# Performance work log

Hardware: AMD Instinct MI355X
Metric: run time of the kernel (lower is better)

Reference implementation:

```python
import jax, jax.numpy as jnp
from jax import lax
import numpy as np

CONF_THRES = 0.55
IOU_THRES = 0.45
MAX_DET = 1000
MAX_WH = 7680.0   # class offset for class-aware NMS (agnostic=False)
K = 4096          # NMS candidate cap (yolov5 max_nms analogue, jit-static)
IMG = 640         # letterboxed network input size
B, N, NC = 16, 25200, 80


def setup_inputs() -> dict:
    key = jax.random.key(0)
    k1, k2, k3, k4 = jax.random.split(key, 4)
    cxcy = jax.random.uniform(k1, (B, N, 2), jnp.float32, 0.0, IMG)
    wh = jax.random.uniform(k2, (B, N, 2), jnp.float32, 2.0, 120.0)
    obj = jax.random.uniform(k3, (B, N, 1), jnp.float32) ** 4
    cls = jax.random.uniform(k4, (B, N, NC), jnp.float32)
    pred = jnp.concatenate([cxcy, wh, obj, cls], axis=-1)  # [B, N, 5+NC]
    return {"pred": pred, "img0_h": 1080, "img0_w": 1920}


def xywh2xyxy(x):
    cx, cy, w, h = x[..., 0], x[..., 1], x[..., 2], x[..., 3]
    return jnp.stack([cx - w / 2, cy - h / 2, cx + w / 2, cy + h / 2], axis=-1)


def box_iou(a, b):
    # a: [K,4], b: [K,4] xyxy -> [K,K]
    lt = jnp.maximum(a[:, None, :2], b[None, :, :2])
    rb = jnp.minimum(a[:, None, 2:], b[None, :, 2:])
    wh = jnp.clip(rb - lt, 0.0)
    inter = wh[..., 0] * wh[..., 1]
    area_a = (a[:, 2] - a[:, 0]) * (a[:, 3] - a[:, 1])
    area_b = (b[:, 2] - b[:, 0]) * (b[:, 3] - b[:, 1])
    return inter / (area_a[:, None] + area_b[None, :] - inter + 1e-7)


def _nms_image(p, img0_h, img0_w):
    # p: [N, 5+NC]
    obj = p[:, 4]
    cls_conf = p[:, 5:] * obj[:, None]          # conf = obj * cls
    conf = cls_conf.max(axis=-1)
    cls_id = cls_conf.argmax(axis=-1)
    valid = (obj > CONF_THRES) & (conf > CONF_THRES)
    score = jnp.where(valid, conf, -1.0)
    # top-K candidates, sorted by confidence (descending)
    top_scores, top_idx = lax.top_k(score, K)
    boxes = xywh2xyxy(p[top_idx, :4])           # [K,4]
    cl = cls_id[top_idx].astype(p.dtype)        # [K]
    iou = box_iou(boxes + cl[:, None] * MAX_WH, boxes + cl[:, None] * MAX_WH)
    idx = jnp.arange(K)
    keep0 = top_scores > 0.0

    def body(i, keep):
        # suppress i if a higher-scoring kept box overlaps it too much
        sup = jnp.any(keep & (idx < i) & (iou[:, i] > IOU_THRES))
        return keep.at[i].set(keep[i] & ~sup)

    keep = lax.fori_loop(0, K, body, keep0)
    kept_score = jnp.where(keep, top_scores, -1.0)
    fs, fi = lax.top_k(kept_score, MAX_DET)
    fb = boxes[fi]                              # [MAX_DET,4]
    fc = cl[fi]
    fvalid = fs > 0.0
    # scale_boxes: letterboxed 640x640 -> original img0
    gain = min(IMG / img0_h, IMG / img0_w)
    pad_x = (IMG - img0_w * gain) / 2
    pad_y = (IMG - img0_h * gain) / 2
    fb = (fb - jnp.array([pad_x, pad_y, pad_x, pad_y], fb.dtype)) / gain
    fb = jnp.clip(fb, 0.0, jnp.array([img0_w, img0_h, img0_w, img0_h], fb.dtype))
    fb = jnp.round(fb)
    det = jnp.concatenate([fb, fs[:, None], fc[:, None]], axis=-1)  # [MAX_DET,6]
    return jnp.where(fvalid[:, None], det, 0.0)


def reference(pred, img0_h, img0_w):
    return jax.vmap(lambda p: _nms_image(p, img0_h, img0_w))(pred)
```

## Files before the change

### kernel.cpp

```cpp
#include <hip/hip_runtime.h>

#define BB 16
#define NN 25200
#define NC 80
#define ROWL 85
#define KTOP 4096
#define MAXDET 1000
#define CONF_T 0.55f
#define IOU_T 0.45f
#define MAX_WH_F 7680.0f
#define CNT_STRIDE 32
#define PCNT_STRIDE 16
#define CCAP 256
#define NBIN 2048

#define OFF_CNT   81920
#define OFF_KCNT  83968
#define OFF_BUCK  86016
#define OFF_KEPT  2707456
#define ZERO_WORDS 21504

__global__ void zero_kernel(unsigned int* __restrict__ w) {
  w[blockIdx.x * 256 + threadIdx.x] = 0u;
}

__global__ __launch_bounds__(256) void score_kernel(const float* __restrict__ pred,
                             unsigned long long* __restrict__ buckets,
                             unsigned int* __restrict__ pcnt,
                             unsigned int* __restrict__ cnt) {
  const int b = blockIdx.y;
  const int lane = threadIdx.x & 63;
  const int a0 = blockIdx.x * 256 + (threadIdx.x & ~63);
  const int a = a0 + lane;
  const int g = lane >> 4;
  const int gl = lane & 15;
  const float* __restrict__ pb = pred + (size_t)b * NN * ROWL;
  float obj = 0.0f;
  if (a < NN) obj = pb[(size_t)a * ROWL + 4];
  unsigned long long mask = __ballot(obj > CONF_T);
  unsigned int nvacc = 0;
  while (mask) {
    int s0 = __ffsll(mask) - 1; mask &= mask - 1;
    int s1 = -1, s2 = -1, s3 = -1;
    if (mask) { s1 = __ffsll(mask) - 1; mask &= mask - 1; }
    if (mask) { s2 = __ffsll(mask) - 1; mask &= mask - 1; }
    if (mask) { s3 = __ffsll(mask) - 1; mask &= mask - 1; }
    const int sg = (g == 0) ? s0 : (g == 1) ? s1 : (g == 2) ? s2 : s3;
    const bool act = (sg >= 0);
    const int srow = act ? sg : s0;
    const int aa = a0 + srow;
    const float objg = __shfl(obj, srow, 64);
    const float* __restrict__ row = pb + (size_t)aa * ROWL;
    float best = -1.0f; int bi = gl;
    #pragma unroll
    for (int t = 0; t < 5; ++t) {
      float v = row[5 + gl + 16 * t] * objg;
      if (v > best) { best = v; bi = gl + 16 * t; }
    }
    #pragma unroll
    for (int off = 1; off <= 8; off <<= 1) {
      float ov = __shfl_xor(best, off, 64);
      int oi = __shfl_xor(bi, off, 64);
      if (ov > best || (ov == best && oi < bi)) { best = ov; bi = oi; }
    }
    bool emit = act && (gl == 0) && (best > CONF_T);
    if (emit) {
      unsigned long long key =
          ((unsigned long long)__float_as_uint(best) << 32) |
          ((unsigned long long)((~(unsigned)aa) & 0xFFFFu) << 16) |
          (unsigned long long)(unsigned)bi;
      unsigned int slot = atomicAdd(&pcnt[(b * NC + bi) * PCNT_STRIDE], 1u);
      if (slot < CCAP)
        buckets[((size_t)(b * NC + bi) << 8) + slot] = key;
    }
    unsigned long long em = __ballot(emit);
    if (lane == 0) nvacc += (unsigned int)__popcll(em);
  }
  if (lane == 0 && nvacc)
    atomicAdd(&cnt[b * CNT_STRIDE], nvacc);
}

__device__ __forceinline__ bool iou_sup(float ax1, float ay1, float ax2, float ay2,
                                        float aar, float bx1, float by1, float bx2,
                                        float by2, float bar) {
  float ltx = fmaxf(ax1, bx1), lty = fmaxf(ay1, by1);
  float rbx = fminf(ax2, bx2), rby = fminf(ay2, by2);
  float wv = rbx - ltx; wv = wv > 0.0f ? wv : 0.0f;
  float hv = rby - lty; hv = hv > 0.0f ? hv : 0.0f;
  float inter = wv * hv;
  float iou = inter / (aar + bar - inter + 1e-7f);
  return iou > IOU_T;
}

__global__ __launch_bounds__(64) void class_nms_kernel(
    const float* __restrict__ pred,
    const unsigned long long* __restrict__ buckets,
    const unsigned int* __restrict__ pcnt,
    const unsigned int* __restrict__ cnt,
    unsigned long long* __restrict__ kept,
    unsigned int* __restrict__ kcnt) {
  const int c = blockIdx.x;
  const int b = blockIdx.y;
  const int lane = threadIdx.x;
  unsigned int pc = pcnt[(b * NC + c) * PCNT_STRIDE];
  int n_c = (int)(pc < (unsigned)CCAP ? pc : (unsigned)CCAP);
  const unsigned long long* __restrict__ bk = buckets + ((size_t)(b * NC + c) << 8);
  const float* __restrict__ pb = pred + (size_t)b * NN * ROWL;
  const float offc = (float)c * MAX_WH_F;
  const int count = (int)cnt[b * CNT_STRIDE];

  if (n_c == 0) return;

  if (n_c <= 64 && count <= KTOP) {
    unsigned long long v0 = (lane < n_c) ? bk[lane] : 0ull;
    for (int k2 = 2; k2 <= 64; k2 <<= 1) {
      for (int j = k2 >> 1; j >= 1; j >>= 1) {
        unsigned long long vo = __shfl_xor(v0, j, 64);
        bool desc = ((lane & k2) == 0);
        bool low = ((lane & j) == 0);
        if ((desc == low) ? (vo > v0) : (vo < v0)) v0 = vo;
      }
    }
    float x1 = 0.f, y1 = 0.f, x2 = 0.f, y2 = 0.f, aar = 0.f;
    const bool inr = (lane < n_c);
    if (inr) {
      unsigned int lo = (unsigned int)v0;
      int aa = (int)((~(lo >> 16)) & 0xFFFFu);
      const float* row = pb + (size_t)aa * ROWL;
      float cx = row[0], cy = row[1], w2 = row[2], h2 = row[3];
      x1 = (cx - w2 / 2.0f) + offc;
      y1 = (cy - h2 / 2.0f) + offc;
      x2 = (cx + w2 / 2.0f) + offc;
      y2 = (cy + h2 / 2.0f) + offc;
      aar = (x2 - x1) * (y2 - y1);
    }
    unsigned long long rowreg = 0ull;
    for (int i2 = 0; i2 < n_c; ++i2) {
      float bx1 = __shfl(x1, i2, 64), by1 = __shfl(y1, i2, 64);
      float bx2 = __shfl(x2, i2, 64), by2 = __shfl(y2, i2, 64);
      float bar = __shfl(aar, i2, 64);
      bool sup = inr && (lane > i2) &&
                 iou_sup(bx1, by1, bx2, by2, bar, x1, y1, x2, y2, aar);
      unsigned long long rm = __ballot(sup);
      if (lane == i2) rowreg = rm;
    }
    unsigned long long cand = (n_c >= 64) ? ~0ull : ((1ull << n_c) - 1ull);
    unsigned long long keepm = 0ull;
    while (cand) {
      int i = __ffsll(cand) - 1;
      keepm |= (1ull << i);
      unsigned long long rowi = __shfl(rowreg, i, 64);
      cand &= ~rowi;
      cand &= ~(1ull << i);
    }
    int keep0 = (int)((keepm >> lane) & 1ull);
    unsigned long long m0 = __ballot(keep0 != 0);
    int tot = (int)__popcll(m0);
    unsigned int base3 = 0;
    if (lane == 0) base3 = atomicAdd(&kcnt[b * CNT_STRIDE], (unsigned int)tot);
    base3 = (unsigned int)__shfl((int)base3, 0, 64);
    if (keep0) {
      unsigned int slot = base3 + (unsigned int)__popcll(m0 & ((1ull << lane) - 1ull));
      if (slot < (unsigned)KTOP) kept[(size_t)b * KTOP + slot] = v0;
    }
    return;
  }

  unsigned long long v[4];
  #pragma unroll
  for (int r = 0; r < 4; ++r) {
    int e = (r << 6) + lane;
    v[r] = (e < n_c) ? bk[e] : 0ull;
  }
  if (count > KTOP) {
    unsigned long long T = 0ull;
    for (int bit = 63; bit >= 0; --bit) {
      unsigned long long T2 = T | (1ull << bit);
      int cge = 0;
      for (int c2 = 0; c2 < NC; ++c2) {
        unsigned int p2 = pcnt[(b * NC + c2) * PCNT_STRIDE];
        int n2 = (int)(p2 < (unsigned)CCAP ? p2 : (unsigned)CCAP);
        const unsigned long long* bk2 = buckets + ((size_t)(b * NC + c2) << 8);
        for (int base2 = 0; base2 < n2; base2 += 64) {
          int i = base2 + lane;
          bool ge = (i < n2) && (bk2[i] >= T2);
          cge += (int)__popcll(__ballot(ge));
        }
      }
      if (cge >= KTOP) T = T2;
    }
    #pragma unroll
    for (int r = 0; r < 4; ++r) if (v[r] < T) v[r] = 0ull;
    n_c = 0;
    #pragma unroll
    for (int r = 0; r < 4; ++r) n_c += (int)__popcll(__ballot(v[r] != 0ull));
    if (n_c == 0) return;
  }
  for (int k2 = 2; k2 <= 256; k2 <<= 1) {
    if (k2 == 256) {
      #pragma unroll
      for (int r = 0; r < 2; ++r) {
        unsigned e = (unsigned)((r << 6) + lane);
        bool desc = ((e & k2) == 0);
        unsigned long long lo_ = v[r], hi_ = v[r + 2];
        bool sw = desc ? (lo_ < hi_) : (lo_ > hi_);
        v[r] = sw ? hi_ : lo_; v[r + 2] = sw ? lo_ : hi_;
      }
    }
    if (k2 >= 128) {
      #pragma unroll
      for (int rr = 0; rr < 2; ++rr) {
        int r = rr * 2;
        unsigned e = (unsigned)((r << 6) + lane);
        bool desc = ((e & k2) == 0);
        unsigned long long lo_ = v[r], hi_ = v[r + 1];
        bool sw = desc ? (lo_ < hi_) : (lo_ > hi_);
        v[r] = sw ? hi_ : lo_; v[r + 1] = sw ? lo_ : hi_;
      }
    }
    int j0 = (k2 >> 1) < 32 ? (k2 >> 1) : 32;
    for (int j = j0; j >= 1; j >>= 1) {
      #pragma unroll
      for (int r = 0; r < 4; ++r) {
        unsigned e = (unsigned)((r << 6) + lane);
        unsigned long long vo = __shfl_xor(v[r], j, 64);
        bool desc = ((e & k2) == 0);
        bool low = ((e & j) == 0);
        if ((desc == low) ? (vo > v[r]) : (vo < v[r])) v[r] = vo;
      }
    }
  }
  float x1r[4], y1r[4], x2r[4], y2r[4], ar[4];
  int keepr[4];
  #pragma unroll
  for (int r = 0; r < 4; ++r) {
    int e = (r << 6) + lane;
    keepr[r] = 0; x1r[r] = 0.f; y1r[r] = 0.f; x2r[r] = 0.f; y2r[r] = 0.f; ar[r] = 0.f;
    if (e < n_c) {
      unsigned int lo = (unsigned int)v[r];
      int aa = (int)((~(lo >> 16)) & 0xFFFFu);
      const float* row = pb + (size_t)aa * ROWL;
      float cx = row[0], cy = row[1], w2 = row[2], h2 = row[3];
      x1r[r] = (cx - w2 / 2.0f) + offc;
      y1r[r] = (cy - h2 / 2.0f) + offc;
      x2r[r] = (cx + w2 / 2.0f) + offc;
      y2r[r] = (cy + h2 / 2.0f) + offc;
      ar[r] = (x2r[r] - x1r[r]) * (y2r[r] - y1r[r]);
      keepr[r] = 1;
    }
  }
  for (int i2 = 0; i2 < n_c; ++i2) {
    int ci = i2 >> 6, li = i2 & 63;
    int ki; float bx1v, by1v, bx2v, by2v, bav;
    #define BCAST(R) { ki = __shfl(keepr[R], li, 64); bx1v = __shfl(x1r[R], li, 64); \
                       by1v = __shfl(y1r[R], li, 64); bx2v = __shfl(x2r[R], li, 64); \
                       by2v = __shfl(y2r[R], li, 64); bav = __shfl(ar[R], li, 64); }
    switch (ci) {
      case 0: BCAST(0); break;
      case 1: BCAST(1); break;
      case 2: BCAST(2); break;
      default: BCAST(3); break;
    }
    #undef BCAST
    if (!ki) continue;
    #pragma unroll
    for (int r = 0; r < 4; ++r) {
      int e = (r << 6) + lane;
      if (keepr[r] && e > i2 &&
          iou_sup(bx1v, by1v, bx2v, by2v, bav, x1r[r], y1r[r], x2r[r], y2r[r], ar[r]))
        keepr[r] = 0;
    }
  }
  unsigned long long m[4];
  int tot = 0;
  #pragma unroll
  for (int r = 0; r < 4; ++r) {
    m[r] = __ballot(keepr[r] != 0);
    tot += (int)__popcll(m[r]);
  }
  unsigned int base3 = 0;
  if (lane == 0) base3 = atomicAdd(&kcnt[b * CNT_STRIDE], (unsigned int)tot);
  base3 = (unsigned int)__shfl((int)base3, 0, 64);
  unsigned int start = base3;
  #pragma unroll
  for (int r = 0; r < 4; ++r) {
    if (keepr[r]) {
      unsigned int slot = start + (unsigned int)__popcll(m[r] & ((1ull << lane) - 1ull));
      if (slot < (unsigned)KTOP) kept[(size_t)b * KTOP + slot] = v[r];
    }
    start += (unsigned int)__popcll(m[r]);
  }
}

__global__ __launch_bounds__(1024) void finalize_kernel(
    const float* __restrict__ pred,
    const unsigned long long* __restrict__ kept,
    const unsigned int* __restrict__ kcnt,
    const int* __restrict__ ihp, const int* __restrict__ iwp,
    float* __restrict__ out) {
  __shared__ unsigned int hist[NBIN];
  __shared__ unsigned int sufx[NBIN];
  __shared__ unsigned int curs[NBIN];
  __shared__ unsigned int scanbuf[1024];
  __shared__ unsigned long long skey[KTOP];
  const int b = blockIdx.x;
  const int tid = threadIdx.x;
  unsigned int kcr = kcnt[b * CNT_STRIDE];
  const int kc = (int)(kcr < (unsigned)KTOP ? kcr : (unsigned)KTOP);
  const unsigned long long* __restrict__ kb = kept + (size_t)b * KTOP;

  for (int i = tid; i < NBIN; i += 1024) hist[i] = 0u;
  __syncthreads();

  unsigned long long myk[4];
  int myb[4];
  #pragma unroll
  for (int r = 0; r < 4; ++r) {
    int i = tid + (r << 10);
    myb[r] = -1; myk[r] = 0ull;
    if (i < kc) {
      unsigned long long k = kb[i];
      int bin = (int)((k >> 44) & (unsigned long long)(NBIN - 1));
      myk[r] = k; myb[r] = bin;
      atomicAdd(&hist[bin], 1u);
    }
  }
  __syncthreads();

  unsigned int h0 = hist[2 * tid], h1 = hist[2 * tid + 1];
  unsigned int val = h0 + h1;
  scanbuf[tid] = val;
  __syncthreads();
  for (int off = 1; off < 1024; off <<= 1) {
    unsigned int add = (tid + off < 1024) ? scanbuf[tid + off] : 0u;
    __syncthreads();
    val += add;
    scanbuf[tid] = val;
    __syncthreads();
  }
  unsigned int excl = val - (h0 + h1);
  sufx[2 * tid] = excl + h1;
  sufx[2 * tid + 1] = excl;
  curs[2 * tid] = excl + h1;
  curs[2 * tid + 1] = excl;
  __syncthreads();

  #pragma unroll
  for (int r = 0; r < 4; ++r) {
    if (myb[r] >= 0) {
      unsigned int p = atomicAdd(&curs[myb[r]], 1u);
      skey[p] = myk[r];
    }
  }
  __syncthreads();

  const int h = ihp[0], w3 = iwp[0];
  const double gd = fmin(640.0 / (double)h, 640.0 / (double)w3);
  const float gain = (float)gd;
  const float padx = (float)((640.0 - (double)w3 * gd) * 0.5);
  const float pady = (float)((640.0 - (double)h * gd) * 0.5);
  const float wf = (float)w3, hf = (float)h;
  #pragma unroll
  for (int r = 0; r < 4; ++r) {
    if (myb[r] >= 0) {
      unsigned long long k = myk[r];
      unsigned int gstart = sufx[myb[r]];
      unsigned int gcnt = hist[myb[r]];
      unsigned int rank = gstart;
      for (unsigned int j = 0; j < gcnt; ++j)
        rank += (skey[gstart + j] > k) ? 1u : 0u;
      if (rank < MAXDET) {
        unsigned int lo = (unsigned int)k;
        int aa = (int)((~(lo >> 16)) & 0xFFFFu);
        int cls = (int)(lo & 0xFFFFu);
        float score = __uint_as_float((unsigned int)(k >> 32));
        const float* row = pred + ((size_t)b * NN + aa) * ROWL;
        float cx = row[0], cy = row[1], wd = row[2], ht = row[3];
        float x1 = cx - wd / 2.0f, y1 = cy - ht / 2.0f;
        float x2 = cx + wd / 2.0f, y2 = cy + ht / 2.0f;
        x1 = rintf(fminf(fmaxf((x1 - padx) / gain, 0.0f), wf));
        y1 = rintf(fminf(fmaxf((y1 - pady) / gain, 0.0f), hf));
        x2 = rintf(fminf(fmaxf((x2 - padx) / gain, 0.0f), wf));
        y2 = rintf(fminf(fmaxf((y2 - pady) / gain, 0.0f), hf));
        float* o = out + ((size_t)b * MAXDET + (int)rank) * 6;
        o[0] = x1; o[1] = y1; o[2] = x2; o[3] = y2;
        o[4] = score; o[5] = (float)cls;
      }
    }
  }
  for (int i = kc + tid; i < MAXDET; i += 1024) {
    float* o = out + ((size_t)b * MAXDET + i) * 6;
    o[0] = 0.0f; o[1] = 0.0f; o[2] = 0.0f; o[3] = 0.0f; o[4] = 0.0f; o[5] = 0.0f;
  }
}

extern "C" void kernel_launch(void* const* d_in, const int* in_sizes, int n_in,
                              void* d_out, int out_size, void* d_ws, size_t ws_size,
                              hipStream_t stream) {
  const float* pred = (const float*)d_in[0];
  const int* ih = (const int*)d_in[1];
  const int* iw = (const int*)d_in[2];
  float* out = (float*)d_out;
  char* ws = (char*)d_ws;

  unsigned int* pcnt = (unsigned int*)ws;
  unsigned int* cnt = (unsigned int*)(ws + OFF_CNT);
  unsigned int* kcnt = (unsigned int*)(ws + OFF_KCNT);
  unsigned long long* buckets = (unsigned long long*)(ws + OFF_BUCK);
  unsigned long long* kept = (unsigned long long*)(ws + OFF_KEPT);

  zero_kernel<<<ZERO_WORDS / 256, 256, 0, stream>>>((unsigned int*)ws);
  dim3 sgrid((NN + 255) / 256, BB);
  score_kernel<<<sgrid, 256, 0, stream>>>(pred, buckets, pcnt, cnt);
  dim3 cgrid(NC, BB);
  class_nms_kernel<<<cgrid, 64, 0, stream>>>(pred, buckets, pcnt, cnt, kept, kcnt);
  finalize_kernel<<<BB, 1024, 0, stream>>>(pred, kept, kcnt, ih, iw, out);
}
```

Measured before the change: 74.15 us.

## Coarsen score and class-NMS blocks, shrink counter padding, use wave-shuffle scan

Each score-kernel wave now handles four 64-anchor segments, so the grid drops to 25 blocks per image. The class NMS kernel packs four classes into one 256-thread block. The per-class counter stride shrinks, which reduces the workspace that must be zeroed. The finalize kernel's barrier-heavy suffix scan is replaced by a wave shuffle scan plus a small cross-wave combine. Together these aim to cut launch and block overhead, zeroing traffic and barrier count, at the cost of less parallelism in the score pass and more atomic contention on counters placed closer together.

```diff
diff --git a/kernel.cpp b/kernel.cpp
--- a/kernel.cpp
+++ b/kernel.cpp
@@ -10,15 +10,15 @@
 #define IOU_T 0.45f
 #define MAX_WH_F 7680.0f
 #define CNT_STRIDE 32
-#define PCNT_STRIDE 16
+#define PCNT_STRIDE 4
 #define CCAP 256
 #define NBIN 2048
 
-#define OFF_CNT   81920
-#define OFF_KCNT  83968
-#define OFF_BUCK  86016
-#define OFF_KEPT  2707456
-#define ZERO_WORDS 21504
+#define OFF_CNT   20480
+#define OFF_KCNT  22528
+#define OFF_BUCK  24576
+#define OFF_KEPT  2646016
+#define ZERO_WORDS 6144
 
 __global__ void zero_kernel(unsigned int* __restrict__ w) {
   w[blockIdx.x * 256 + threadIdx.x] = 0u;
@@ -30,51 +30,56 @@
                              unsigned int* __restrict__ cnt) {
   const int b = blockIdx.y;
   const int lane = threadIdx.x & 63;
-  const int a0 = blockIdx.x * 256 + (threadIdx.x & ~63);
-  const int a = a0 + lane;
+  const int w = threadIdx.x >> 6;
   const int g = lane >> 4;
   const int gl = lane & 15;
   const float* __restrict__ pb = pred + (size_t)b * NN * ROWL;
-  float obj = 0.0f;
-  if (a < NN) obj = pb[(size_t)a * ROWL + 4];
-  unsigned long long mask = __ballot(obj > CONF_T);
   unsigned int nvacc = 0;
-  while (mask) {
-    int s0 = __ffsll(mask) - 1; mask &= mask - 1;
-    int s1 = -1, s2 = -1, s3 = -1;
-    if (mask) { s1 = __ffsll(mask) - 1; mask &= mask - 1; }
-    if (mask) { s2 = __ffsll(mask) - 1; mask &= mask - 1; }
-    if (mask) { s3 = __ffsll(mask) - 1; mask &= mask - 1; }
-    const int sg = (g == 0) ? s0 : (g == 1) ? s1 : (g == 2) ? s2 : s3;
-    const bool act = (sg >= 0);
-    const int srow = act ? sg : s0;
-    const int aa = a0 + srow;
-    const float objg = __shfl(obj, srow, 64);
-    const float* __restrict__ row = pb + (size_t)aa * ROWL;
-    float best = -1.0f; int bi = gl;
-    #pragma unroll
-    for (int t = 0; t < 5; ++t) {
-      float v = row[5 + gl + 16 * t] * objg;
-      if (v > best) { best = v; bi = gl + 16 * t; }
-    }
-    #pragma unroll
-    for (int off = 1; off <= 8; off <<= 1) {
-      float ov = __shfl_xor(best, off, 64);
-      int oi = __shfl_xor(bi, off, 64);
-      if (ov > best || (ov == best && oi < bi)) { best = ov; bi = oi; }
-    }
-    bool emit = act && (gl == 0) && (best > CONF_T);
-    if (emit) {
-      unsigned long long key =
-          ((unsigned long long)__float_as_uint(best) << 32) |
-          ((unsigned long long)((~(unsigned)aa) & 0xFFFFu) << 16) |
-          (unsigned long long)(unsigned)bi;
-      unsigned int slot = atomicAdd(&pcnt[(b * NC + bi) * PCNT_STRIDE], 1u);
-      if (slot < CCAP)
-        buckets[((size_t)(b * NC + bi) << 8) + slot] = key;
-    }
-    unsigned long long em = __ballot(emit);
-    if (lane == 0) nvacc += (unsigned int)__popcll(em);
+  for (int t = 0; t < 4; ++t) {
+    const int seg = blockIdx.x * 16 + w * 4 + t;
+    const int a0 = seg * 64;
+    if (a0 >= NN) break;
+    const int a = a0 + lane;
+    float obj = 0.0f;
+    if (a < NN) obj = pb[(size_t)a * ROWL + 4];
+    unsigned long long mask = __ballot(obj > CONF_T);
+    while (mask) {
+      int s0 = __ffsll(mask) - 1; mask &= mask - 1;
+      int s1 = -1, s2 = -1, s3 = -1;
+      if (mask) { s1 = __ffsll(mask) - 1; mask &= mask - 1; }
+      if (mask) { s2 = __ffsll(mask) - 1; mask &= mask - 1; }
+      if (mask) { s3 = __ffsll(mask) - 1; mask &= mask - 1; }
+      const int sg = (g == 0) ? s0 : (g == 1) ? s1 : (g == 2) ? s2 : s3;
+      const bool act = (sg >= 0);
+      const int srow = act ? sg : s0;
+      const int aa = a0 + srow;
+      const float objg = __shfl(obj, srow, 64);
+      const float* __restrict__ row = pb + (size_t)aa * ROWL;
+      float best = -1.0f; int bi = gl;
+      #pragma unroll
+      for (int u = 0; u < 5; ++u) {
+        float v = row[5 + gl + 16 * u] * objg;
+        if (v > best) { best = v; bi = gl + 16 * u; }
+      }
+      #pragma unroll
+      for (int off = 1; off <= 8; off <<= 1) {
+        float ov = __shfl_xor(best, off, 64);
+        int oi = __shfl_xor(bi, off, 64);
+        if (ov > best || (ov == best && oi < bi)) { best = ov; bi = oi; }
+      }
+      bool emit = act && (gl == 0) && (best > CONF_T);
+      if (emit) {
+        unsigned long long key =
+            ((unsigned long long)__float_as_uint(best) << 32) |
+            ((unsigned long long)((~(unsigned)aa) & 0xFFFFu) << 16) |
+            (unsigned long long)(unsigned)bi;
+        unsigned int slot = atomicAdd(&pcnt[(b * NC + bi) * PCNT_STRIDE], 1u);
+        if (slot < CCAP)
+          buckets[((size_t)(b * NC + bi) << 8) + slot] = key;
+      }
+      unsigned long long em = __ballot(emit);
+      if (lane == 0) nvacc += (unsigned int)__popcll(em);
+    }
   }
   if (lane == 0 && nvacc)
     atomicAdd(&cnt[b * CNT_STRIDE], nvacc);
@@ -92,16 +97,16 @@
   return iou > IOU_T;
 }
 
-__global__ __launch_bounds__(64) void class_nms_kernel(
+__global__ __launch_bounds__(256) void class_nms_kernel(
     const float* __restrict__ pred,
     const unsigned long long* __restrict__ buckets,
     const unsigned int* __restrict__ pcnt,
     const unsigned int* __restrict__ cnt,
     unsigned long long* __restrict__ kept,
     unsigned int* __restrict__ kcnt) {
-  const int c = blockIdx.x;
+  const int c = blockIdx.x * 4 + (threadIdx.x >> 6);
   const int b = blockIdx.y;
-  const int lane = threadIdx.x;
+  const int lane = threadIdx.x & 63;
   unsigned int pc = pcnt[(b * NC + c) * PCNT_STRIDE];
   int n_c = (int)(pc < (unsigned)CCAP ? pc : (unsigned)CCAP);
   const unsigned long long* __restrict__ bk = buckets + ((size_t)(b * NC + c) << 8);
@@ -301,15 +306,17 @@
   __shared__ unsigned int hist[NBIN];
   __shared__ unsigned int sufx[NBIN];
   __shared__ unsigned int curs[NBIN];
-  __shared__ unsigned int scanbuf[1024];
+  __shared__ unsigned int wsum[16], woff[16];
   __shared__ unsigned long long skey[KTOP];
   const int b = blockIdx.x;
   const int tid = threadIdx.x;
+  const int lane = tid & 63;
+  const int w = tid >> 6;
   unsigned int kcr = kcnt[b * CNT_STRIDE];
   const int kc = (int)(kcr < (unsigned)KTOP ? kcr : (unsigned)KTOP);
   const unsigned long long* __restrict__ kb = kept + (size_t)b * KTOP;
 
-  for (int i = tid; i < NBIN; i += 1024) hist[i] = 0u;
+  hist[2 * tid] = 0u; hist[2 * tid + 1] = 0u;
   __syncthreads();
 
   unsigned long long myk[4];
@@ -328,17 +335,22 @@
   __syncthreads();
 
   unsigned int h0 = hist[2 * tid], h1 = hist[2 * tid + 1];
-  unsigned int val = h0 + h1;
-  scanbuf[tid] = val;
-  __syncthreads();
-  for (int off = 1; off < 1024; off <<= 1) {
-    unsigned int add = (tid + off < 1024) ? scanbuf[tid + off] : 0u;
-    __syncthreads();
-    val += add;
-    scanbuf[tid] = val;
-    __syncthreads();
-  }
-  unsigned int excl = val - (h0 + h1);
+  unsigned int v = h0 + h1;
+  #pragma unroll
+  for (int off = 1; off < 64; off <<= 1) {
+    unsigned int o = __shfl_down(v, off, 64);
+    if (lane + off < 64) v += o;
+  }
+  if (lane == 0) wsum[w] = v;
+  __syncthreads();
+  if (tid < 16) {
+    unsigned int s = 0;
+    for (int j = tid + 1; j < 16; ++j) s += wsum[j];
+    woff[tid] = s;
+  }
+  __syncthreads();
+  unsigned int incl = v + woff[w];
+  unsigned int excl = incl - (h0 + h1);
   sufx[2 * tid] = excl + h1;
   sufx[2 * tid + 1] = excl;
   curs[2 * tid] = excl + h1;
@@ -410,9 +422,9 @@
   unsigned long long* kept = (unsigned long long*)(ws + OFF_KEPT);
 
   zero_kernel<<<ZERO_WORDS / 256, 256, 0, stream>>>((unsigned int*)ws);
-  dim3 sgrid((NN + 255) / 256, BB);
+  dim3 sgrid(25, BB);
   score_kernel<<<sgrid, 256, 0, stream>>>(pred, buckets, pcnt, cnt);
-  dim3 cgrid(NC, BB);
-  class_nms_kernel<<<cgrid, 64, 0, stream>>>(pred, buckets, pcnt, cnt, kept, kcnt);
+  dim3 cgrid(NC / 4, BB);
+  class_nms_kernel<<<cgrid, 256, 0, stream>>>(pred, buckets, pcnt, cnt, kept, kcnt);
   finalize_kernel<<<BB, 1024, 0, stream>>>(pred, kept, kcnt, ih, iw, out);
 }
```

Result: slower. 82.16 us (+10.8%).
